# Optimization experiments

Measured on AMD Instinct MI355X. Metric: run time of the kernel, lower is better.

The kernel has to match this reference:

```python
import jax, jax.numpy as jnp
import numpy as np

EPS_BN = 1e-5
CLAMP_MAX = 1e-10  # nn.Hardtanh(min_val=0, max_val=1e-10) on squared dists


def _three_nn(xyz1, xyz2):
    # xyz1: (b, n, 3), xyz2: (b, m, 3) -> sq dists (b, n, 3), idx (b, n, 3)
    d2 = (jnp.sum(xyz1 ** 2, -1, keepdims=True)
          - 2.0 * jnp.einsum('bnc,bmc->bnm', xyz1, xyz2)
          + jnp.sum(xyz2 ** 2, -1)[:, None, :])  # (b, n, m)
    neg, idx = jax.lax.top_k(-d2, 3)
    return -neg, idx


def _conv_bn_relu(x, W, b, g, beta):
    # x: (b, n, cin); 1x1 Conv2d == pointwise linear, BN over (batch, spatial)
    y = jnp.einsum('bnc,oc->bno', x, W) + b
    mean = jnp.mean(y, axis=(0, 1))
    var = jnp.mean((y - mean) ** 2, axis=(0, 1))
    y = (y - mean) * jax.lax.rsqrt(var + EPS_BN) * g + beta
    return jax.nn.relu(y)


def setup_inputs() -> dict:
    key = jax.random.key(0)
    ks = jax.random.split(key, 8)
    b, n, m, c1, c2 = 16, 4096, 1024, 256, 512
    mlp, dimin = [256, 256], [c1 + c2, 256]
    inp = {
        'xyz1': jax.random.normal(ks[0], (b, n, 3), jnp.float32),
        'xyz2': jax.random.normal(ks[1], (b, m, 3), jnp.float32),
        'points1': jax.random.normal(ks[2], (b, n, c1), jnp.float32),
        'points2': jax.random.normal(ks[3], (b, m, c2), jnp.float32),
        'W1': jax.random.normal(ks[4], (mlp[0], dimin[0]), jnp.float32) * 0.02,
        'b1': jnp.zeros((mlp[0],), jnp.float32),
        'g1': jnp.ones((mlp[0],), jnp.float32),
        'beta1': jnp.zeros((mlp[0],), jnp.float32),
        'W2': jax.random.normal(ks[5], (mlp[1], dimin[1]), jnp.float32) * 0.02,
        'b2': jnp.zeros((mlp[1],), jnp.float32),
        'g2': jnp.ones((mlp[1],), jnp.float32),
        'beta2': jnp.zeros((mlp[1],), jnp.float32),
    }
    return inp


def reference(xyz1, xyz2, points1, points2, W1, b1, g1, beta1, W2, b2, g2, beta2):
    dist, idx = _three_nn(xyz1, xyz2)                     # (b, n, 3)
    dist = jnp.clip(dist, 0.0, CLAMP_MAX)                 # Hardtanh(0, 1e-10)
    inv = 1.0 / dist
    weight = inv / jnp.sum(inv, axis=2, keepdims=True)    # (b, n, 3)
    neigh = jax.vmap(lambda p, i: p[i])(points2, idx)     # (b, n, 3, c2)
    interp = jnp.einsum('bnk,bnkc->bnc', weight, neigh)   # (b, n, c2)
    feat = jnp.concatenate([interp, points1], axis=2)     # (b, n, c2+c1)
    feat = _conv_bn_relu(feat, W1, b1, g1, beta1)
    feat = _conv_bn_relu(feat, W2, b2, g2, beta2)
    return jnp.transpose(feat, (0, 2, 1))                 # (b, c_out, n)
```

## Files before the change

### kernel.cpp

```cpp
#include <hip/hip_runtime.h>

typedef unsigned short u16;
typedef short sh8 __attribute__((ext_vector_type(8)));
typedef float floatx4 __attribute__((ext_vector_type(4)));
typedef float float4v __attribute__((ext_vector_type(4)));
typedef u16 us8 __attribute__((ext_vector_type(8)));
typedef u16 us4 __attribute__((ext_vector_type(4)));

#define NB    16
#define NPTS  4096
#define MPTS  1024
#define CC1   256
#define CC2   512
#define KK1   768
#define CCO   256
#define MT    (NB*NPTS)
#define MZ    (NB*MPTS)

__device__ __forceinline__ float b2f(u16 u) {
    union { unsigned i; float f; } v; v.i = ((unsigned)u) << 16; return v.f;
}
__device__ __forceinline__ u16 f2b(float f) {
    union { float f; unsigned i; } v; v.f = f;
    unsigned u = v.i;
    unsigned r = (u + 0x7fffu + ((u >> 16) & 1u)) >> 16;
    return (u16)r;
}
__device__ __forceinline__ float ldv(const void* p, size_t i, int f32) {
    return f32 ? ((const float*)p)[i] : b2f(((const u16*)p)[i]);
}
__device__ __forceinline__ void stv(void* p, size_t i, int f32, float v) {
    if (f32) ((float*)p)[i] = v; else ((u16*)p)[i] = f2b(v);
}
__device__ __forceinline__ void gl_lds16(const void* g, void* l) {
    __builtin_amdgcn_global_load_lds(
        (const __attribute__((address_space(1))) void*)g,
        (__attribute__((address_space(3))) void*)l, 16, 0, 0);
}

__global__ void Pointnet_fp_module_33071248179394_kernel(
        const unsigned* g1bits, int* flag, float* stats) {
    int i = blockIdx.x * 256 + threadIdx.x;
    stats[i] = 0.f;
    if (i == 0) flag[0] = (g1bits[0] == 0x3F800000u) ? 1 : 0;
}

__global__ __launch_bounds__(512) void three_nn_k(
        const int* flagp, const void* xyz1, const void* xyz2,
        int* nidx, float* nw) {
    __shared__ float4 P[MPTS];
    __shared__ float md[512][3];
    __shared__ int   mi[512][3];
    const int f32 = flagp[0];
    const int bi = blockIdx.x >> 6;
    const int chunk = blockIdx.x & 63;
    const int t = threadIdx.x;
    const int ql = t & 63, sp = t >> 6;

    for (int p = t; p < MPTS; p += 512) {
        size_t s = (size_t)(bi * MPTS + p) * 3;
        P[p] = make_float4(ldv(xyz2, s, f32), ldv(xyz2, s + 1, f32),
                           ldv(xyz2, s + 2, f32), 0.f);
    }
    __syncthreads();

    const int q = chunk * 64 + ql;
    size_t s1 = (size_t)(bi * NPTS + q) * 3;
    const float qx = ldv(xyz1, s1 + 0, f32);
    const float qy = ldv(xyz1, s1 + 1, f32);
    const float qz = ldv(xyz1, s1 + 2, f32);

    float d0 = 3e38f, d1 = 3e38f, dv2 = 3e38f;
    int i0 = -1, i1 = -1, i2 = -1;
    const int jbeg = sp * 128, jend = jbeg + 128;
    #pragma unroll 4
    for (int j = jbeg; j < jend; j++) {
        float4 p = P[j];
        float dx = qx - p.x;
        float dy = qy - p.y;
        float dz = qz - p.z;
        float dd = fmaf(dx, dx, fmaf(dy, dy, dz * dz));
        if (dd < dv2) {
            if (dd < d0)      { dv2 = d1; i2 = i1; d1 = d0; i1 = i0; d0 = dd; i0 = j; }
            else if (dd < d1) { dv2 = d1; i2 = i1; d1 = dd; i1 = j; }
            else              { dv2 = dd; i2 = j; }
        }
    }
    md[t][0] = d0;  md[t][1] = d1;  md[t][2] = dv2;
    mi[t][0] = i0;  mi[t][1] = i1;  mi[t][2] = i2;
    __syncthreads();

    if (t < 64) {
        float b0 = 3e38f, b1 = 3e38f, b2v = 3e38f;
        int j0 = -1, j1 = -1, j2 = -1;
        #pragma unroll
        for (int s = 0; s < 8; s++) {
            int base = s * 64 + t;
            #pragma unroll
            for (int k = 0; k < 3; k++) {
                float d = md[base][k];
                int ji = mi[base][k];
                if (d < b0)      { b2v = b1; j2 = j1; b1 = b0; j1 = j0; b0 = d; j0 = ji; }
                else if (d < b1) { b2v = b1; j2 = j1; b1 = d; j1 = ji; }
                else if (d < b2v){ b2v = d; j2 = ji; }
            }
        }
        float e0 = fminf(fmaxf(b0, 0.f), 1e-10f);
        float e1 = fminf(fmaxf(b1, 0.f), 1e-10f);
        float e2 = fminf(fmaxf(b2v, 0.f), 1e-10f);
        float v0 = 1.0f / e0, v1 = 1.0f / e1, v2 = 1.0f / e2;
        float s = v0 + v1 + v2;
        const size_t gq = ((size_t)bi * NPTS + chunk * 64 + t) * 3;
        nidx[gq + 0] = j0; nidx[gq + 1] = j1; nidx[gq + 2] = j2;
        nw[gq + 0] = v0 / s; nw[gq + 1] = v1 / s; nw[gq + 2] = v2 / s;
    }
}

__global__ __launch_bounds__(256) void cvt_w_k(
        const int* flagp, const void* W1, const void* W2,
        u16* Wa, u16* Wbp, u16* W2b) {
    const int f32 = flagp[0];
    const int i = blockIdx.x * 256 + threadIdx.x;
    if (i < CCO * CC2) {
        int r = i >> 9, c = i & 511;
        Wa[i] = f2b(ldv(W1, (size_t)r * KK1 + c, f32));
    } else if (i < CCO * CC2 + CCO * CC1) {
        int k = i - CCO * CC2;
        int r = k >> 8, c = k & 255;
        Wbp[k] = f2b(ldv(W1, (size_t)r * KK1 + CC2 + c, f32));
    } else {
        int k = i - CCO * CC2 - CCO * CC1;
        W2b[k] = f2b(ldv(W2, k, f32));
    }
}

__global__ __launch_bounds__(256) void cvt_pts_k(
        const int* flagp, const void* p2, const void* p1,
        u16* p2b, u16* p1b) {
    const int f32 = flagp[0];
    size_t i = ((size_t)blockIdx.x * 256 + threadIdx.x) * 8;
    const size_t N2 = (size_t)MZ * CC2;
    const void* src; u16* dst; size_t off;
    if (i < N2) { src = p2; dst = p2b; off = i; }
    else        { src = p1; dst = p1b; off = i - N2; }
    us8 o;
    if (f32) {
        float4v a = *(const float4v*)((const float*)src + off);
        float4v b = *(const float4v*)((const float*)src + off + 4);
        #pragma unroll
        for (int k = 0; k < 4; k++) { o[k] = f2b(a[k]); o[k + 4] = f2b(b[k]); }
    } else {
        o = *(const us8*)((const u16*)src + off);
    }
    *(us8*)(dst + off) = o;
}

template<int K, int NW, bool STATS, bool BN1>
__global__ __launch_bounds__(128 * NW, 2) void gemm_bt(
        const int* flagp, const u16* __restrict__ A, const u16* __restrict__ B,
        const void* __restrict__ bias, u16* __restrict__ Y,
        float* __restrict__ sum, float* __restrict__ sq,
        const float* __restrict__ nsum, const float* __restrict__ nsq,
        const void* __restrict__ ng, const void* __restrict__ nbeta) {
    constexpr int T  = 128 * NW;
    constexpr int NT = NW * 64;
    __shared__ u16 As[128 * 32];
    __shared__ u16 Bs[NT * 32];
    __shared__ float sSum[STATS ? NT : 1], sSq[STATS ? NT : 1];
    __shared__ float ssc[BN1 ? 256 : 1], ssh[BN1 ? 256 : 1];
    const int f32 = flagp[0];
    const int tid = threadIdx.x;
    const int m0 = blockIdx.x * 128;
    const int n0 = blockIdx.y * NT;
    const int wave = tid >> 6, lane = tid & 63;
    const int wm = wave & 1, wn = wave >> 1;
    const int l16 = lane & 15, quad = lane >> 4;

    if (STATS && tid < NT) { sSum[tid] = 0.f; sSq[tid] = 0.f; }
    if (BN1 && tid < 256) {
        const float invM = 1.0f / (float)MT;
        float mean = nsum[tid] * invM;
        float var = nsq[tid] * invM - mean * mean;
        float sc = rsqrtf(var + 1e-5f) * ldv(ng, tid, f32);
        ssc[tid] = sc;
        ssh[tid] = ldv(nbeta, tid, f32) - mean * sc;
    }

    floatx4 acc[4][4];
    #pragma unroll
    for (int i = 0; i < 4; i++)
        #pragma unroll
        for (int j = 0; j < 4; j++)
            acc[i][j] = (floatx4){0.f, 0.f, 0.f, 0.f};

    for (int kb = 0; kb < K; kb += 32) {
        __syncthreads();
        #pragma unroll
        for (int c = tid; c < 512; c += T) {
            int row = c >> 2, c4 = c & 3;
            if (BN1) {
                us8 a = *(const us8*)(A + (size_t)(m0 + row) * K + kb + c4 * 8);
                us8 o;
                #pragma unroll
                for (int k = 0; k < 8; k++) {
                    int ch = kb + c4 * 8 + k;
                    o[k] = f2b(fmaxf(b2f((u16)a[k]) * ssc[ch] + ssh[ch], 0.f));
                }
                *(us8*)(As + c * 8) = o;
            } else {
                gl_lds16(A + (size_t)(m0 + row) * K + kb + c4 * 8, As + c * 8);
            }
        }
        #pragma unroll
        for (int c = tid; c < NT * 4; c += T) {
            int row = c >> 2, c4 = c & 3;
            gl_lds16(B + (size_t)(n0 + row) * K + kb + c4 * 8, Bs + c * 8);
        }
        __syncthreads();

        sh8 af[4], bfr[4];
        #pragma unroll
        for (int i = 0; i < 4; i++)
            af[i] = *(const sh8*)(As + (wm * 64 + i * 16 + l16) * 32 + quad * 8);
        #pragma unroll
        for (int j = 0; j < 4; j++)
            bfr[j] = *(const sh8*)(Bs + (wn * 64 + j * 16 + l16) * 32 + quad * 8);
        #pragma unroll
        for (int i = 0; i < 4; i++)
            #pragma unroll
            for (int j = 0; j < 4; j++)
                acc[i][j] = __builtin_amdgcn_mfma_f32_16x16x32_bf16(
                                bfr[j], af[i], acc[i][j], 0, 0, 0);
    }

    float bvv[4][4];
    #pragma unroll
    for (int j = 0; j < 4; j++)
        #pragma unroll
        for (int r = 0; r < 4; r++) {
            int col = n0 + wn * 64 + j * 16 + quad * 4 + r;
            bvv[j][r] = bias ? ldv(bias, col, f32) : 0.f;
        }

    float cs[4][4], css[4][4];
    if (STATS) {
        #pragma unroll
        for (int j = 0; j < 4; j++)
            #pragma unroll
            for (int r = 0; r < 4; r++) { cs[j][r] = 0.f; css[j][r] = 0.f; }
    }

    #pragma unroll
    for (int i = 0; i < 4; i++) {
        int row = m0 + wm * 64 + i * 16 + l16;
        #pragma unroll
        for (int j = 0; j < 4; j++) {
            int colb = wn * 64 + j * 16 + quad * 4;
            us4 o;
            #pragma unroll
            for (int r = 0; r < 4; r++) {
                float v = acc[i][j][r] + bvv[j][r];
                if (STATS) { cs[j][r] += v; css[j][r] += v * v; }
                o[r] = f2b(v);
            }
            *(us4*)(Y + (size_t)row * CCO + n0 + colb) = o;
        }
    }
    if (STATS) {
        #pragma unroll
        for (int j = 0; j < 4; j++)
            #pragma unroll
            for (int r = 0; r < 4; r++) {
                float a = cs[j][r], b = css[j][r];
                #pragma unroll
                for (int m = 1; m < 16; m <<= 1) {
                    a += __shfl_xor(a, m, 64);
                    b += __shfl_xor(b, m, 64);
                }
                if (l16 == 0) {
                    int cl = wn * 64 + j * 16 + quad * 4 + r;
                    atomicAdd(&sSum[cl], a);
                    atomicAdd(&sSq[cl], b);
                }
            }
        __syncthreads();
        if (tid < NT) {
            atomicAdd(&sum[n0 + tid], sSum[tid]);
            atomicAdd(&sq[n0 + tid], sSq[tid]);
        }
    }
}

__global__ __launch_bounds__(512, 2) void gemm_p_k(
        const int* flagp, const u16* __restrict__ A, const u16* __restrict__ B,
        const void* __restrict__ bias, const int* __restrict__ nidx,
        const float* __restrict__ nw, const u16* __restrict__ Z,
        u16* __restrict__ Y, float* __restrict__ sum, float* __restrict__ sq) {
    __shared__ u16 As[128 * 32];
    __shared__ u16 Bs[256 * 32];
    __shared__ int   sIdx[128 * 3];
    __shared__ float sW[128 * 3];
    __shared__ float sSum[256], sSq[256];
    const int f32 = flagp[0];
    const int tid = threadIdx.x;
    const int m0 = blockIdx.x * 128;
    const int wave = tid >> 6, lane = tid & 63;
    const int wm = wave & 1, wn = wave >> 1;
    const int l16 = lane & 15, quad = lane >> 4;
    const int zbase = (m0 >> 12) << 10;

    if (tid < 128) {
        size_t q3 = (size_t)(m0 + tid) * 3;
        #pragma unroll
        for (int k = 0; k < 3; k++) {
            sIdx[tid * 3 + k] = nidx[q3 + k];
            sW[tid * 3 + k]   = nw[q3 + k];
        }
    }
    if (tid < 256) { sSum[tid] = 0.f; sSq[tid] = 0.f; }

    floatx4 acc[4][4];
    #pragma unroll
    for (int i = 0; i < 4; i++)
        #pragma unroll
        for (int j = 0; j < 4; j++)
            acc[i][j] = (floatx4){0.f, 0.f, 0.f, 0.f};

    constexpr int K = 256;
    for (int kb = 0; kb < K; kb += 32) {
        __syncthreads();
        {
            int row = tid >> 2, c4 = tid & 3;
            gl_lds16(A + (size_t)(m0 + row) * K + kb + c4 * 8, As + tid * 8);
        }
        #pragma unroll
        for (int c = tid; c < 1024; c += 512) {
            int row = c >> 2, c4 = c & 3;
            gl_lds16(B + (size_t)row * K + kb + c4 * 8, Bs + c * 8);
        }
        __syncthreads();

        sh8 af[4], bfr[4];
        #pragma unroll
        for (int i = 0; i < 4; i++)
            af[i] = *(const sh8*)(As + (wm * 64 + i * 16 + l16) * 32 + quad * 8);
        #pragma unroll
        for (int j = 0; j < 4; j++)
            bfr[j] = *(const sh8*)(Bs + (wn * 64 + j * 16 + l16) * 32 + quad * 8);
        #pragma unroll
        for (int i = 0; i < 4; i++)
            #pragma unroll
            for (int j = 0; j < 4; j++)
                acc[i][j] = __builtin_amdgcn_mfma_f32_16x16x32_bf16(
                                bfr[j], af[i], acc[i][j], 0, 0, 0);
    }

    float bvv[4][4];
    #pragma unroll
    for (int j = 0; j < 4; j++)
        #pragma unroll
        for (int r = 0; r < 4; r++)
            bvv[j][r] = ldv(bias, wn * 64 + j * 16 + quad * 4 + r, f32);

    float cs[4][4], css[4][4];
    #pragma unroll
    for (int j = 0; j < 4; j++)
        #pragma unroll
        for (int r = 0; r < 4; r++) { cs[j][r] = 0.f; css[j][r] = 0.f; }

    #pragma unroll
    for (int i = 0; i < 4; i++) {
        int rl = wm * 64 + i * 16 + l16;
        int i0 = sIdx[rl * 3 + 0], i1 = sIdx[rl * 3 + 1], i2 = sIdx[rl * 3 + 2];
        float w0 = sW[rl * 3 + 0], w1 = sW[rl * 3 + 1], w2 = sW[rl * 3 + 2];
        const u16* z0 = Z + (size_t)(zbase + i0) * CCO;
        const u16* z1 = Z + (size_t)(zbase + i1) * CCO;
        const u16* z2 = Z + (size_t)(zbase + i2) * CCO;
        u16* yrow = Y + (size_t)(m0 + rl) * CCO;
        #pragma unroll
        for (int j = 0; j < 4; j++) {
            int colb = wn * 64 + j * 16 + quad * 4;
            us4 zv0 = *(const us4*)(z0 + colb);
            us4 zv1 = *(const us4*)(z1 + colb);
            us4 zv2 = *(const us4*)(z2 + colb);
            us4 o;
            #pragma unroll
            for (int r = 0; r < 4; r++) {
                float v = acc[i][j][r] + bvv[j][r]
                        + w0 * b2f((u16)zv0[r]) + w1 * b2f((u16)zv1[r])
                        + w2 * b2f((u16)zv2[r]);
                cs[j][r] += v; css[j][r] += v * v;
                o[r] = f2b(v);
            }
            *(us4*)(yrow + colb) = o;
        }
    }
    #pragma unroll
    for (int j = 0; j < 4; j++)
        #pragma unroll
        for (int r = 0; r < 4; r++) {
            float a = cs[j][r], b = css[j][r];
            #pragma unroll
            for (int m = 1; m < 16; m <<= 1) {
                a += __shfl_xor(a, m, 64);
                b += __shfl_xor(b, m, 64);
            }
            if (l16 == 0) {
                int cl = wn * 64 + j * 16 + quad * 4 + r;
                atomicAdd(&sSum[cl], a);
                atomicAdd(&sSq[cl], b);
            }
        }
    __syncthreads();
    if (tid < 256) {
        atomicAdd(&sum[tid], sSum[tid]);
        atomicAdd(&sq[tid], sSq[tid]);
    }
}

__global__ void bn_out_k(const int* flagp, const u16* Y, void* Out,
                         const float* sum, const float* sq,
                         const void* g, const void* beta) {
    __shared__ float tile[64][65];
    const int f32 = flagp[0];
    const int bi = blockIdx.z;
    const int p0 = blockIdx.x * 64;
    const int c0 = blockIdx.y * 64;
    const int t = threadIdx.x;
    const int cr = t & 63, rq = t >> 6;
    const float invM = 1.0f / (float)MT;

    const int c = c0 + cr;
    float mean = sum[c] * invM;
    float var = sq[c] * invM - mean * mean;
    float sc = rsqrtf(var + 1e-5f) * ldv(g, c, f32);
    float sh = ldv(beta, c, f32) - mean * sc;

    for (int r = rq; r < 64; r += 4) {
        int m = bi * NPTS + p0 + r;
        float v = b2f(Y[(size_t)m * CCO + c]) * sc + sh;
        tile[r][cr] = fmaxf(v, 0.f);
    }
    __syncthreads();
    for (int r = rq; r < 64; r += 4) {
        size_t o = ((size_t)bi * CCO + (c0 + r)) * NPTS + p0 + cr;
        stv(Out, o, f32, tile[cr][r]);
    }
}

extern "C" void kernel_launch(void* const* d_in, const int* in_sizes, int n_in,
                              void* d_out, int out_size, void* d_ws, size_t ws_size,
                              hipStream_t stream) {
    const void* xyz1    = d_in[0];
    const void* xyz2    = d_in[1];
    const void* points1 = d_in[2];
    const void* points2 = d_in[3];
    const void* W1      = d_in[4];
    const void* b1      = d_in[5];
    const void* g1      = d_in[6];
    const void* be1     = d_in[7];
    const void* W2      = d_in[8];
    const void* b2      = d_in[9];
    const void* g2      = d_in[10];
    const void* be2     = d_in[11];
    char* ws = (char*)d_ws;

    int*   flag  = (int*)(ws + 0);
    float* sum1  = (float*)(ws + 4096);
    float* sq1   = (float*)(ws + 5120);
    float* sum2  = (float*)(ws + 6144);
    float* sq2   = (float*)(ws + 7168);
    int*   nidx  = (int*)(ws + 20480);
    float* nw    = (float*)(ws + 806912);
    u16* Wa   = (u16*)(ws + 2097152);
    u16* Wbp  = (u16*)(ws + 2359296);
    u16* W2b  = (u16*)(ws + 2490368);
    u16* Z    = (u16*)(ws + 2621440);
    u16* p2b  = (u16*)(ws + 11010048ULL);
    u16* p1b  = (u16*)(ws + 27787264ULL);
    u16* y1   = (u16*)(ws + 61341696ULL);
    u16* y2   = (u16*)(ws + 94896128ULL);

    Pointnet_fp_module_33071248179394_kernel<<<dim3(16), dim3(256), 0, stream>>>(
        (const unsigned*)g1, flag, (float*)(ws + 4096));
    cvt_w_k<<<dim3(1024), dim3(256), 0, stream>>>(
        flag, W1, W2, Wa, Wbp, W2b);
    cvt_pts_k<<<dim3((MZ * CC2 + MT * CC1) / 2048), dim3(256), 0, stream>>>(
        flag, points2, points1, p2b, p1b);
    three_nn_k<<<dim3(1024), dim3(512), 0, stream>>>(flag, xyz1, xyz2, nidx, nw);
    gemm_bt<CC2, 2, false, false><<<dim3(MZ / 128, 2), dim3(256), 0, stream>>>(
        flag, p2b, Wa, nullptr, Z, nullptr, nullptr,
        nullptr, nullptr, nullptr, nullptr);
    gemm_p_k<<<dim3(MT / 128), dim3(512), 0, stream>>>(
        flag, p1b, Wbp, b1, nidx, nw, Z, y1, sum1, sq1);
    gemm_bt<CCO, 4, true, true><<<dim3(MT / 128, 1), dim3(512), 0, stream>>>(
        flag, y1, W2b, b2, y2, sum2, sq2,
        sum1, sq1, g1, be1);
    bn_out_k<<<dim3(64, 4, NB), dim3(256), 0, stream>>>(
        flag, y2, d_out, sum2, sq2, g2, be2);
}
```

Baseline: 324.5 us.

## Stage full-K A tile in swizzled LDS, read B directly from global

The two K=256 GEMMs (gather+points1 and layer 2 with fused BN1+ReLU) now share one templated kernel. It loads the whole 128x256 A tile once into XOR-swizzled LDS and reads weight fragments straight from global/L2. This removes the per-K-step LDS staging and barriers, and the swizzle is meant to avoid LDS bank conflicts. The trade-off is 64KB of LDS per block, which likely limits occupancy despite launch_bounds of 4, and uncached global B reads inside the MFMA loop.

After: 331.2 us. 1.02x slower.

```diff
diff --git a/kernel.cpp b/kernel.cpp
--- a/kernel.cpp
+++ b/kernel.cpp
@@ -155,20 +155,14 @@
     *(us8*)(dst + off) = o;
 }
 
-template<int K, int NW, bool STATS, bool BN1>
-__global__ __launch_bounds__(128 * NW, 2) void gemm_bt(
+template<int K, int NW>
+__global__ __launch_bounds__(128 * NW, 2) void gemm_z_k(
         const int* flagp, const u16* __restrict__ A, const u16* __restrict__ B,
-        const void* __restrict__ bias, u16* __restrict__ Y,
-        float* __restrict__ sum, float* __restrict__ sq,
-        const float* __restrict__ nsum, const float* __restrict__ nsq,
-        const void* __restrict__ ng, const void* __restrict__ nbeta) {
+        u16* __restrict__ Y) {
     constexpr int T  = 128 * NW;
     constexpr int NT = NW * 64;
     __shared__ u16 As[128 * 32];
     __shared__ u16 Bs[NT * 32];
-    __shared__ float sSum[STATS ? NT : 1], sSq[STATS ? NT : 1];
-    __shared__ float ssc[BN1 ? 256 : 1], ssh[BN1 ? 256 : 1];
-    const int f32 = flagp[0];
     const int tid = threadIdx.x;
     const int m0 = blockIdx.x * 128;
     const int n0 = blockIdx.y * NT;
@@ -176,16 +170,6 @@
     const int wm = wave & 1, wn = wave >> 1;
     const int l16 = lane & 15, quad = lane >> 4;
 
-    if (STATS && tid < NT) { sSum[tid] = 0.f; sSq[tid] = 0.f; }
-    if (BN1 && tid < 256) {
-        const float invM = 1.0f / (float)MT;
-        float mean = nsum[tid] * invM;
-        float var = nsq[tid] * invM - mean * mean;
-        float sc = rsqrtf(var + 1e-5f) * ldv(ng, tid, f32);
-        ssc[tid] = sc;
-        ssh[tid] = ldv(nbeta, tid, f32) - mean * sc;
-    }
-
     floatx4 acc[4][4];
     #pragma unroll
     for (int i = 0; i < 4; i++)
@@ -198,18 +182,7 @@
         #pragma unroll
         for (int c = tid; c < 512; c += T) {
             int row = c >> 2, c4 = c & 3;
-            if (BN1) {
-                us8 a = *(const us8*)(A + (size_t)(m0 + row) * K + kb + c4 * 8);
-                us8 o;
-                #pragma unroll
-                for (int k = 0; k < 8; k++) {
-                    int ch = kb + c4 * 8 + k;
-                    o[k] = f2b(fmaxf(b2f((u16)a[k]) * ssc[ch] + ssh[ch], 0.f));
-                }
-                *(us8*)(As + c * 8) = o;
-            } else {
-                gl_lds16(A + (size_t)(m0 + row) * K + kb + c4 * 8, As + c * 8);
-            }
+            gl_lds16(A + (size_t)(m0 + row) * K + kb + c4 * 8, As + c * 8);
         }
         #pragma unroll
         for (int c = tid; c < NT * 4; c += T) {
@@ -233,23 +206,6 @@
                                 bfr[j], af[i], acc[i][j], 0, 0, 0);
     }
 
-    float bvv[4][4];
-    #pragma unroll
-    for (int j = 0; j < 4; j++)
-        #pragma unroll
-        for (int r = 0; r < 4; r++) {
-            int col = n0 + wn * 64 + j * 16 + quad * 4 + r;
-            bvv[j][r] = bias ? ldv(bias, col, f32) : 0.f;
-        }
-
-    float cs[4][4], css[4][4];
-    if (STATS) {
-        #pragma unroll
-        for (int j = 0; j < 4; j++)
-            #pragma unroll
-            for (int r = 0; r < 4; r++) { cs[j][r] = 0.f; css[j][r] = 0.f; }
-    }
-
     #pragma unroll
     for (int i = 0; i < 4; i++) {
         int row = m0 + wm * 64 + i * 16 + l16;
@@ -258,58 +214,45 @@
             int colb = wn * 64 + j * 16 + quad * 4;
             us4 o;
             #pragma unroll
-            for (int r = 0; r < 4; r++) {
-                float v = acc[i][j][r] + bvv[j][r];
-                if (STATS) { cs[j][r] += v; css[j][r] += v * v; }
-                o[r] = f2b(v);
-            }
+            for (int r = 0; r < 4; r++)
+                o[r] = f2b(acc[i][j][r]);
             *(us4*)(Y + (size_t)row * CCO + n0 + colb) = o;
         }
     }
-    if (STATS) {
-        #pragma unroll
-        for (int j = 0; j < 4; j++)
-            #pragma unroll
-            for (int r = 0; r < 4; r++) {
-                float a = cs[j][r], b = css[j][r];
-                #pragma unroll
-                for (int m = 1; m < 16; m <<= 1) {
-                    a += __shfl_xor(a, m, 64);
-                    b += __shfl_xor(b, m, 64);
-                }
-                if (l16 == 0) {
-                    int cl = wn * 64 + j * 16 + quad * 4 + r;
-                    atomicAdd(&sSum[cl], a);
-                    atomicAdd(&sSq[cl], b);
-                }
-            }
-        __syncthreads();
-        if (tid < NT) {
-            atomicAdd(&sum[n0 + tid], sSum[tid]);
-            atomicAdd(&sq[n0 + tid], sSq[tid]);
-        }
-    }
-}
-
-__global__ __launch_bounds__(512, 2) void gemm_p_k(
+}
+
+template<bool GATHER, bool BN1>
+__global__ __launch_bounds__(512, 4) void gemm_mt_k(
         const int* flagp, const u16* __restrict__ A, const u16* __restrict__ B,
         const void* __restrict__ bias, const int* __restrict__ nidx,
         const float* __restrict__ nw, const u16* __restrict__ Z,
-        u16* __restrict__ Y, float* __restrict__ sum, float* __restrict__ sq) {
-    __shared__ u16 As[128 * 32];
-    __shared__ u16 Bs[256 * 32];
-    __shared__ int   sIdx[128 * 3];
-    __shared__ float sW[128 * 3];
+        u16* __restrict__ Y, float* __restrict__ sum, float* __restrict__ sq,
+        const float* __restrict__ nsum, const float* __restrict__ nsq,
+        const void* __restrict__ ng, const void* __restrict__ nbeta) {
+    __shared__ u16 As[128 * 256];
     __shared__ float sSum[256], sSq[256];
+    __shared__ int   sIdx[GATHER ? 384 : 1];
+    __shared__ float sW[GATHER ? 384 : 1];
+    __shared__ float ssc[BN1 ? 256 : 1], ssh[BN1 ? 256 : 1];
     const int f32 = flagp[0];
     const int tid = threadIdx.x;
     const int m0 = blockIdx.x * 128;
     const int wave = tid >> 6, lane = tid & 63;
     const int wm = wave & 1, wn = wave >> 1;
     const int l16 = lane & 15, quad = lane >> 4;
-    const int zbase = (m0 >> 12) << 10;
-
-    if (tid < 128) {
+
+    if (tid < 256) {
+        sSum[tid] = 0.f; sSq[tid] = 0.f;
+        if (BN1) {
+            const float invM = 1.0f / (float)MT;
+            float mean = nsum[tid] * invM;
+            float var = nsq[tid] * invM - mean * mean;
+            float sc = rsqrtf(var + 1e-5f) * ldv(ng, tid, f32);
+            ssc[tid] = sc;
+            ssh[tid] = ldv(nbeta, tid, f32) - mean * sc;
+        }
+    }
+    if (GATHER && tid < 128) {
         size_t q3 = (size_t)(m0 + tid) * 3;
         #pragma unroll
         for (int k = 0; k < 3; k++) {
@@ -317,7 +260,26 @@
             sW[tid * 3 + k]   = nw[q3 + k];
         }
     }
-    if (tid < 256) { sSum[tid] = 0.f; sSq[tid] = 0.f; }
+    if (BN1) __syncthreads();
+
+    #pragma unroll
+    for (int c = tid; c < 4096; c += 512) {
+        int r = c >> 5, cp = c & 31;
+        int col = ((cp ^ (r & 7)) << 3);
+        if (BN1) {
+            us8 a = *(const us8*)(A + (size_t)(m0 + r) * 256 + col);
+            us8 o;
+            #pragma unroll
+            for (int k = 0; k < 8; k++) {
+                int ch = col + k;
+                o[k] = f2b(fmaxf(b2f((u16)a[k]) * ssc[ch] + ssh[ch], 0.f));
+            }
+            *(us8*)(As + c * 8) = o;
+        } else {
+            gl_lds16(A + (size_t)(m0 + r) * 256 + col, As + c * 8);
+        }
+    }
+    __syncthreads();
 
     floatx4 acc[4][4];
     #pragma unroll
@@ -326,27 +288,19 @@
         for (int j = 0; j < 4; j++)
             acc[i][j] = (floatx4){0.f, 0.f, 0.f, 0.f};
 
-    constexpr int K = 256;
-    for (int kb = 0; kb < K; kb += 32) {
-        __syncthreads();
-        {
-            int row = tid >> 2, c4 = tid & 3;
-            gl_lds16(A + (size_t)(m0 + row) * K + kb + c4 * 8, As + tid * 8);
-        }
-        #pragma unroll
-        for (int c = tid; c < 1024; c += 512) {
-            int row = c >> 2, c4 = c & 3;
-            gl_lds16(B + (size_t)row * K + kb + c4 * 8, Bs + c * 8);
-        }
-        __syncthreads();
-
+    #pragma unroll 2
+    for (int kb = 0; kb < 256; kb += 32) {
         sh8 af[4], bfr[4];
         #pragma unroll
-        for (int i = 0; i < 4; i++)
-            af[i] = *(const sh8*)(As + (wm * 64 + i * 16 + l16) * 32 + quad * 8);
-        #pragma unroll
         for (int j = 0; j < 4; j++)
-            bfr[j] = *(const sh8*)(Bs + (wn * 64 + j * 16 + l16) * 32 + quad * 8);
+            bfr[j] = *(const sh8*)(B + (size_t)(wn * 64 + j * 16 + l16) * 256
+                                     + kb + quad * 8);
+        #pragma unroll
+        for (int i = 0; i < 4; i++) {
+            int r = wm * 64 + i * 16 + l16;
+            int cp = ((kb >> 3) + quad) ^ (l16 & 7);
+            af[i] = *(const sh8*)(As + r * 256 + (cp << 3));
+        }
         #pragma unroll
         for (int i = 0; i < 4; i++)
             #pragma unroll
@@ -368,29 +322,43 @@
         #pragma unroll
         for (int r = 0; r < 4; r++) { cs[j][r] = 0.f; css[j][r] = 0.f; }
 
+    const int zbase = GATHER ? ((m0 >> 12) << 10) : 0;
     #pragma unroll
     for (int i = 0; i < 4; i++) {
         int rl = wm * 64 + i * 16 + l16;
-        int i0 = sIdx[rl * 3 + 0], i1 = sIdx[rl * 3 + 1], i2 = sIdx[rl * 3 + 2];
-        float w0 = sW[rl * 3 + 0], w1 = sW[rl * 3 + 1], w2 = sW[rl * 3 + 2];
-        const u16* z0 = Z + (size_t)(zbase + i0) * CCO;
-        const u16* z1 = Z + (size_t)(zbase + i1) * CCO;
-        const u16* z2 = Z + (size_t)(zbase + i2) * CCO;
+        const u16 *z0 = nullptr, *z1 = nullptr, *z2 = nullptr;
+        float w0 = 0.f, w1 = 0.f, w2 = 0.f;
+        if (GATHER) {
+            int i0 = sIdx[rl * 3 + 0], i1 = sIdx[rl * 3 + 1], i2 = sIdx[rl * 3 + 2];
+            w0 = sW[rl * 3 + 0]; w1 = sW[rl * 3 + 1]; w2 = sW[rl * 3 + 2];
+            z0 = Z + (size_t)(zbase + i0) * CCO;
+            z1 = Z + (size_t)(zbase + i1) * CCO;
+            z2 = Z + (size_t)(zbase + i2) * CCO;
+        }
         u16* yrow = Y + (size_t)(m0 + rl) * CCO;
         #pragma unroll
         for (int j = 0; j < 4; j++) {
             int colb = wn * 64 + j * 16 + quad * 4;
-            us4 zv0 = *(const us4*)(z0 + colb);
-            us4 zv1 = *(const us4*)(z1 + colb);
-            us4 zv2 = *(const us4*)(z2 + colb);
             us4 o;
-            #pragma unroll
-            for (int r = 0; r < 4; r++) {
-                float v = acc[i][j][r] + bvv[j][r]
-                        + w0 * b2f((u16)zv0[r]) + w1 * b2f((u16)zv1[r])
-                        + w2 * b2f((u16)zv2[r]);
-                cs[j][r] += v; css[j][r] += v * v;
-                o[r] = f2b(v);
+            if (GATHER) {
+                us4 zv0 = *(const us4*)(z0 + colb);
+                us4 zv1 = *(const us4*)(z1 + colb);
+                us4 zv2 = *(const us4*)(z2 + colb);
+                #pragma unroll
+                for (int r = 0; r < 4; r++) {
+                    float v = acc[i][j][r] + bvv[j][r]
+                            + w0 * b2f((u16)zv0[r]) + w1 * b2f((u16)zv1[r])
+                            + w2 * b2f((u16)zv2[r]);
+                    cs[j][r] += v; css[j][r] += v * v;
+                    o[r] = f2b(v);
+                }
+            } else {
+                #pragma unroll
+                for (int r = 0; r < 4; r++) {
+                    float v = acc[i][j][r] + bvv[j][r];
+                    cs[j][r] += v; css[j][r] += v * v;
+                    o[r] = f2b(v);
+                }
             }
             *(us4*)(yrow + colb) = o;
         }
@@ -488,13 +456,13 @@
     cvt_pts_k<<<dim3((MZ * CC2 + MT * CC1) / 2048), dim3(256), 0, stream>>>(
         flag, points2, points1, p2b, p1b);
     three_nn_k<<<dim3(1024), dim3(512), 0, stream>>>(flag, xyz1, xyz2, nidx, nw);
-    gemm_bt<CC2, 2, false, false><<<dim3(MZ / 128, 2), dim3(256), 0, stream>>>(
-        flag, p2b, Wa, nullptr, Z, nullptr, nullptr,
+    gemm_z_k<CC2, 2><<<dim3(MZ / 128, 2), dim3(256), 0, stream>>>(
+        flag, p2b, Wa, Z);
+    gemm_mt_k<true, false><<<dim3(MT / 128), dim3(512), 0, stream>>>(
+        flag, p1b, Wbp, b1, nidx, nw, Z, y1, sum1, sq1,
         nullptr, nullptr, nullptr, nullptr);
-    gemm_p_k<<<dim3(MT / 128), dim3(512), 0, stream>>>(
-        flag, p1b, Wbp, b1, nidx, nw, Z, y1, sum1, sq1);
-    gemm_bt<CCO, 4, true, true><<<dim3(MT / 128, 1), dim3(512), 0, stream>>>(
-        flag, y1, W2b, b2, y2, sum2, sq2,
+    gemm_mt_k<false, true><<<dim3(MT / 128), dim3(512), 0, stream>>>(
+        flag, y1, W2b, b2, nullptr, nullptr, nullptr, y2, sum2, sq2,
         sum1, sq1, g1, be1);
     bn_out_k<<<dim3(64, 4, NB), dim3(256), 0, stream>>>(
         flag, y2, d_out, sum2, sq2, g2, be2);
```
